# Kernel tuning notes

Measured on AMD Instinct MI355X. Metric: run time of the kernel, lower is better.

## Reference

```python
import jax, jax.numpy as jnp
import numpy as np
from jax import lax


def _conv(x, W, b):
    # x: [B,C,H,W], W: [O,I,3,3] -> [B,O,H,W], SAME padding, stride 1
    y = lax.conv_general_dilated(x, W, window_strides=(1, 1), padding='SAME',
                                 dimension_numbers=('NCHW', 'OIHW', 'NCHW'))
    return y + b[None, :, None, None]


def _cell(x, h, c, W, b):
    # Standard ConvLSTMCell: conv(concat(x,h)) -> 4*Hd gate channels (i,f,o,g)
    gates = _conv(jnp.concatenate([x, h], axis=1), W, b)
    ci, cf, co, cg = jnp.split(gates, 4, axis=1)
    i = jax.nn.sigmoid(ci)
    f = jax.nn.sigmoid(cf)
    o = jax.nn.sigmoid(co)
    g = jnp.tanh(cg)
    c_next = f * c + i * g
    h_next = o * jnp.tanh(c_next)
    return h_next, c_next


def setup_inputs() -> dict:
    key = jax.random.key(0)
    ks = jax.random.split(key, 4)
    B, T, C, H, W = 1, 32, 4, 128, 128
    Hd = 64
    x = jax.random.normal(ks[0], (B, T, C, H, W), dtype=jnp.float32)
    # small init scale to keep sigmoid/tanh out of deep saturation
    W0 = jax.random.normal(ks[1], (4 * Hd, C + Hd, 3, 3), dtype=jnp.float32) * 0.05
    b0 = jnp.zeros((4 * Hd,), dtype=jnp.float32)
    W1 = jax.random.normal(ks[2], (4 * Hd, Hd + Hd, 3, 3), dtype=jnp.float32) * 0.05
    b1 = jnp.zeros((4 * Hd,), dtype=jnp.float32)
    Wr = jax.random.normal(ks[3], (1, Hd, 3, 3), dtype=jnp.float32) * 0.05
    br = jnp.zeros((1,), dtype=jnp.float32)
    return {"x": x, "W0": W0, "b0": b0, "W1": W1, "b1": b1, "Wr": Wr, "br": br}


def reference(x, W0, b0, W1, b1, Wr, br):
    # Train mode with epsilon=1 (deterministic teacher forcing), hidden_state=None
    B, T, C, H, Wd = x.shape
    Hd = Wr.shape[1]
    zeros = jnp.zeros((B, Hd, H, Wd), dtype=x.dtype)
    carry0 = (zeros, zeros, zeros, zeros)  # (h0, c0, h1, c1)

    def step(carry, x_t):
        h0, c0, h1, c1 = carry
        h0, c0 = _cell(x_t, h0, c0, W0, b0)
        h1, c1 = _cell(h0, h1, c1, W1, b1)
        y = _conv(h1, Wr, br)  # [B,1,H,W]
        return (h0, c0, h1, c1), y[0]  # squeeze batch dim (B=1) -> [1,H,W]

    xs = jnp.transpose(x, (1, 0, 2, 3, 4))  # [T,B,C,H,W]
    _, ys = lax.scan(step, carry0, xs)
    return ys  # [T,1,H,W]
```

## Files before the change

kernel.cpp:

```cpp
#include <hip/hip_runtime.h>
#include <cstdint>
#include <cmath>

#define HW 128
#define NPIX (HW * HW)

typedef _Float16 half8 __attribute__((ext_vector_type(8)));
typedef _Float16 half4 __attribute__((ext_vector_type(4)));
typedef float floatx16 __attribute__((ext_vector_type(16)));
typedef unsigned long long u64;

__device__ __forceinline__ float sigf(float x) {
    return __builtin_amdgcn_rcpf(1.0f + __expf(-x));
}
__device__ __forceinline__ float tanhf_(float x) {
    float cx = fminf(fmaxf(x, -20.0f), 20.0f);
    float e2 = __expf(2.0f * cx);
    return (e2 - 1.0f) * __builtin_amdgcn_rcpf(e2 + 1.0f);
}

__device__ __forceinline__ half8 ld_coh(const _Float16* p) {
    union { u64 u[2]; half8 h; } cv;
    cv.u[0] = __hip_atomic_load((const u64*)p,
                                __ATOMIC_RELAXED, __HIP_MEMORY_SCOPE_AGENT);
    cv.u[1] = __hip_atomic_load((const u64*)p + 1,
                                __ATOMIC_RELAXED, __HIP_MEMORY_SCOPE_AGENT);
    return cv.h;
}

__device__ __forceinline__ void st_coh8(_Float16* p, half4 v) {
    asm volatile("global_store_dwordx2 %0, %1, off sc0 sc1"
                 :: "v"(p), "v"(v) : "memory");
}
__device__ __forceinline__ void st_coh4(float* p, float v) {
    asm volatile("global_store_dword %0, %1, off sc0 sc1"
                 :: "v"(p), "v"(v) : "memory");
}

__device__ __forceinline__ void group_sync(unsigned* gcnt, int g,
                                           int gy, int gx, unsigned k)
{
    asm volatile("s_waitcnt vmcnt(0)" ::: "memory");
    __syncthreads();
    const int tid = threadIdx.x;
    if (tid == 0)
        __hip_atomic_fetch_add(gcnt + g * 16, 1u,
                               __ATOMIC_RELAXED, __HIP_MEMORY_SCOPE_AGENT);
    if (tid < 9) {
        int dy = tid / 3 - 1, dx = tid % 3 - 1;
        int gy2 = gy + dy, gx2 = gx + dx;
        if (gy2 >= 0 && gy2 < 8 && gx2 >= 0 && gx2 < 4) {
            const unsigned* p = gcnt + (gy2 * 4 + gx2) * 16;
            while (__hip_atomic_load(p, __ATOMIC_RELAXED,
                                     __HIP_MEMORY_SCOPE_AGENT) < 8u * k)
                __builtin_amdgcn_s_sleep(1);
        }
    }
    __syncthreads();
}

template<int NKC, int CELL>
__device__ __forceinline__ void cell_phase(
    const _Float16* __restrict__ xt,
    const _Float16* __restrict__ hA,
    const _Float16* __restrict__ hB,
    const _Float16* wlds,
    const float* blds,
    float (&cr)[2][4],
    _Float16* __restrict__ hOut,
    _Float16* sbuf,
    const int (&spb)[3], const int (&slo)[3], int ch16,
    int y0, int x0, int s)
{
    const int tid  = threadIdx.x;
    const int lane = tid & 63;
    const int w    = tid >> 6;
    const int cl   = lane & 31;
    const int l5   = lane >> 5;

    half8 regs[NKC][3];
    #pragma unroll
    for (int kc = 0; kc < NKC; ++kc) {
        #pragma unroll
        for (int e0 = 0; e0 < 3; ++e0) {
            half8 v = {0, 0, 0, 0, 0, 0, 0, 0};
            const int pb = spb[e0];
            if (pb >= 0) {
                if (CELL == 0) {
                    if (kc == 0) { if (ch16 == 0) v = *(const half8*)(xt + (pb >> 3)); }
                    else v = ld_coh(hA + pb + (kc - 1) * 16);
                } else {
                    v = (kc < 4) ? ld_coh(hA + pb + kc * 16)
                                 : ld_coh(hB + pb + (kc - 4) * 16);
                }
            }
            regs[kc][e0] = v;
        }
    }

    floatx16 acc[2];
    #pragma unroll
    for (int p_ = 0; p_ < 2; ++p_)
        #pragma unroll
        for (int i = 0; i < 16; ++i) acc[p_][i] = 0.0f;

    __syncthreads();
    #pragma unroll
    for (int e0 = 0; e0 < 3; ++e0)
        if (slo[e0] >= 0) *(half8*)(sbuf + slo[e0]) = regs[0][e0];
    __syncthreads();

    const int r0 = 2 * w;
    #pragma unroll
    for (int kc = 0; kc < NKC; ++kc) {
        const _Float16* wk = wlds + (size_t)(kc * 9) * 512 + lane * 8;
        const _Float16* bbase = sbuf + ((size_t)((kc & 1) * 2 + l5) * 612) * 8;

        half8 bufA[3], bufB[3];
        #pragma unroll
        for (int d = 0; d < 3; ++d) {
            bufA[d] = *(const half8*)(bbase + ((r0    ) * 34 + cl + d) * 8);
            bufB[d] = *(const half8*)(bbase + ((r0 + 1) * 34 + cl + d) * 8);
        }
        #pragma unroll
        for (int dx = 0; dx < 3; ++dx) {
            half8 a = *(const half8*)(wk + dx * 512);
            acc[0] = __builtin_amdgcn_mfma_f32_32x32x16_f16(a, bufA[dx], acc[0], 0, 0, 0);
            acc[1] = __builtin_amdgcn_mfma_f32_32x32x16_f16(a, bufB[dx], acc[1], 0, 0, 0);
        }
        #pragma unroll
        for (int d = 0; d < 3; ++d)
            bufA[d] = *(const half8*)(bbase + ((r0 + 2) * 34 + cl + d) * 8);
        #pragma unroll
        for (int dx = 0; dx < 3; ++dx) {
            half8 a = *(const half8*)(wk + (3 + dx) * 512);
            acc[0] = __builtin_amdgcn_mfma_f32_32x32x16_f16(a, bufB[dx], acc[0], 0, 0, 0);
            acc[1] = __builtin_amdgcn_mfma_f32_32x32x16_f16(a, bufA[dx], acc[1], 0, 0, 0);
        }
        #pragma unroll
        for (int d = 0; d < 3; ++d)
            bufB[d] = *(const half8*)(bbase + ((r0 + 3) * 34 + cl + d) * 8);
        #pragma unroll
        for (int dx = 0; dx < 3; ++dx) {
            half8 a = *(const half8*)(wk + (6 + dx) * 512);
            acc[0] = __builtin_amdgcn_mfma_f32_32x32x16_f16(a, bufA[dx], acc[0], 0, 0, 0);
            acc[1] = __builtin_amdgcn_mfma_f32_32x32x16_f16(a, bufB[dx], acc[1], 0, 0, 0);
        }

        if (kc + 1 < NKC) {
            const int b = (kc + 1) & 1;
            #pragma unroll
            for (int e0 = 0; e0 < 3; ++e0)
                if (slo[e0] >= 0)
                    *(half8*)(sbuf + b * 9792 + slo[e0]) = regs[kc + 1][e0];
        }
        __syncthreads();
    }

    #pragma unroll
    for (int pos = 0; pos < 2; ++pos) {
        const int p  = 2 * w + pos;
        const int px = (y0 + p) * HW + x0 + cl;
        half4 hn;
        #pragma unroll
        for (int j = 0; j < 4; ++j) {
            const int bo = CELL * 32 + 4 * l5 + j;
            float iv = sigf(acc[pos][     j] + blds[bo]);
            float fv = sigf(acc[pos][ 4 + j] + blds[bo + 8]);
            float ov = sigf(acc[pos][ 8 + j] + blds[bo + 16]);
            float gv = tanhf_(acc[pos][12 + j] + blds[bo + 24]);
            float cv = fv * cr[pos][j] + iv * gv;
            cr[pos][j] = cv;
            hn[j] = (_Float16)(ov * tanhf_(cv));
        }
        st_coh8(hOut + (size_t)px * 64 + s * 8 + 4 * l5, hn);
    }
}

__device__ __forceinline__ void readout_phase(
    const half8 (&rv)[2], const float* wl, float brv,
    float* __restrict__ yout, _Float16* sbuf,
    const int (&rlo)[2], int yidx)
{
    const int tid = threadIdx.x;
    __syncthreads();
    #pragma unroll
    for (int e0 = 0; e0 < 2; ++e0)
        if (rlo[e0] >= 0) *(half8*)(sbuf + rlo[e0]) = rv[e0];
    __syncthreads();

    const int sub = tid & 7;
    const int p   = tid >> 3;
    const int pr  = p >> 3, pcc = p & 7;
    float sacc = 0.0f;
    #pragma unroll
    for (int dy = 0; dy < 3; ++dy)
        #pragma unroll
        for (int dx = 0; dx < 3; ++dx) {
            int pc = (pr + dy) * 10 + (pcc + dx);
            half8 hv = *(const half8*)(sbuf + ((size_t)pc * 8 + sub) * 8);
            int tap = dy * 3 + dx;
            #pragma unroll
            for (int j = 0; j < 8; ++j)
                sacc += wl[(sub * 8 + j) * 9 + tap] * (float)hv[j];
        }
    sacc += __shfl_xor(sacc, 1);
    sacc += __shfl_xor(sacc, 2);
    sacc += __shfl_xor(sacc, 4);
    if (sub == 0) st_coh4(yout + yidx, sacc + brv);
}

__global__ __launch_bounds__(512, 2)
void mega(const _Float16* __restrict__ xh, const _Float16* __restrict__ WpG,
          const float* __restrict__ b0g, const float* __restrict__ b1g,
          const float* __restrict__ Wr, const float* __restrict__ br,
          _Float16* __restrict__ h0a, _Float16* __restrict__ h0b,
          _Float16* __restrict__ h1a, _Float16* __restrict__ h1b,
          float* __restrict__ y, unsigned* gcnt)
{
    extern __shared__ __align__(16) char dyn[];
    _Float16* wlds = (_Float16*)dyn;
    _Float16* sbuf = (_Float16*)(dyn + 119808);
    float*    wl   = (float*)(dyn + 158976);
    float*    blds = (float*)(dyn + 161280);

    const int tid = threadIdx.x;
    const int bid = blockIdx.x;
    const int s = bid >> 5, g = bid & 31;
    const int ggy = g >> 2, ggx = g & 3;
    const int y0 = ggy * 16, x0 = ggx * 32;

    const half8* wsrc = (const half8*)(WpG + (size_t)s * 59904);
    for (int i = tid; i < 7488; i += 512) ((half8*)wlds)[i] = wsrc[i];
    for (int i = tid; i < 576; i += 512) wl[i] = Wr[i];
    if (tid < 64) {
        int cell = tid >> 5, gj = tid & 31;
        int gate = gj >> 3, h8 = gj & 7;
        blds[tid] = (cell ? b1g : b0g)[gate * 64 + s * 8 + h8];
    }
    const float brv = br[0];
    float c0r[2][4] = {{0, 0, 0, 0}, {0, 0, 0, 0}};
    float c1r[2][4] = {{0, 0, 0, 0}, {0, 0, 0, 0}};

    const int ch16 = tid & 1;
    int spb[3], slo[3];
    #pragma unroll
    for (int e0 = 0; e0 < 3; ++e0) {
        int e = tid + e0 * 512;
        spb[e0] = -1; slo[e0] = -1;
        if (e < 1224) {
            int pc = e >> 1;
            int r = pc / 34, c = pc - r * 34;
            int gy = y0 - 1 + r, gx = x0 - 1 + c;
            slo[e0] = (ch16 * 612 + pc) * 8;
            if (gy >= 0 && gy < HW && gx >= 0 && gx < HW)
                spb[e0] = (gy * HW + gx) * 64 + ch16 * 8;
        }
    }
    const int ch8 = tid & 7;
    const int py0 = y0 + (s >> 2) * 8, px0 = x0 + (s & 3) * 8;
    int rpb[2], rlo[2];
    #pragma unroll
    for (int e0 = 0; e0 < 2; ++e0) {
        int e = tid + e0 * 512;
        rpb[e0] = -1; rlo[e0] = -1;
        if (e < 800) {
            int pc = e >> 3;
            int r = pc / 10, c = pc - r * 10;
            int gy = py0 - 1 + r, gx = px0 - 1 + c;
            rlo[e0] = (pc * 8 + ch8) * 8;
            if (gy >= 0 && gy < HW && gx >= 0 && gx < HW)
                rpb[e0] = (gy * HW + gx) * 64 + ch8 * 8;
        }
    }
    const int yidx = (py0 + ((tid >> 3) >> 3)) * HW + px0 + ((tid >> 3) & 7);

    __syncthreads();

    #pragma unroll 1
    for (int t = 0; t < 32; ++t) {
        const _Float16* xt = xh + (size_t)t * NPIX * 8;
        _Float16* h0r = (t & 1) ? h0b : h0a;
        _Float16* h0w = (t & 1) ? h0a : h0b;
        _Float16* h1r = (t & 1) ? h1b : h1a;
        _Float16* h1w = (t & 1) ? h1a : h1b;

        cell_phase<5, 0>(xt, h0r, nullptr, wlds, blds, c0r, h0w, sbuf,
                         spb, slo, ch16, y0, x0, s);
        group_sync(gcnt, g, ggy, ggx, (unsigned)(t + 1));

        half8 rv[2];
        #pragma unroll
        for (int e0 = 0; e0 < 2; ++e0) {
            half8 v = {0, 0, 0, 0, 0, 0, 0, 0};
            if (rpb[e0] >= 0) v = ld_coh(h1r + rpb[e0]);
            rv[e0] = v;
        }

        cell_phase<8, 1>(nullptr, h0w, h1r, wlds + 23040, blds, c1r, h1w, sbuf,
                         spb, slo, ch16, y0, x0, s);
        if (t > 0) readout_phase(rv, wl, brv, y + (size_t)(t - 1) * NPIX, sbuf,
                                 rlo, yidx);
    }
    group_sync(gcnt, g, ggy, ggx, 33u);
    {
        half8 rv[2];
        #pragma unroll
        for (int e0 = 0; e0 < 2; ++e0) {
            half8 v = {0, 0, 0, 0, 0, 0, 0, 0};
            if (rpb[e0] >= 0) v = ld_coh(h1a + rpb[e0]);
            rv[e0] = v;
        }
        readout_phase(rv, wl, brv, y + (size_t)31 * NPIX, sbuf, rlo, yidx);
    }
}

__global__ void pack_w(const float* __restrict__ W, _Float16* __restrict__ Wp,
                       int NKC, int CIN_W, int cell1, int base, int total)
{
    int idx = blockIdx.x * 256 + threadIdx.x;
    if (idx >= total) return;
    int j = idx & 7, l = (idx >> 3) & 63;
    int rest = idx >> 9;
    int tap = rest % 9;
    int kt  = rest / 9;
    int kc = kt % NKC, s = kt / NKC;
    int rr = l & 31, l5 = l >> 5;
    int o = (rr >> 3) * 64 + s * 8 + (rr & 7);
    int k = kc * 16 + l5 * 8 + j;
    int cin = cell1 ? ((k < 4) ? k : ((k >= 16 && k < 80) ? k - 12 : -1)) : k;
    float v = (cin >= 0) ? W[((size_t)o * CIN_W + cin) * 9 + tap] : 0.0f;
    Wp[(size_t)s * 59904 + base + (size_t)(kc * 9 + tap) * 512 + l * 8 + j] = (_Float16)v;
}

__global__ void xconv(const float* __restrict__ x, _Float16* __restrict__ xh)
{
    int idx = blockIdx.x * 256 + threadIdx.x;
    int t = idx >> 14, px = idx & 16383;
    const float* xs = x + (size_t)t * 4 * NPIX + px;
    half8 v = {0, 0, 0, 0, 0, 0, 0, 0};
    v[0] = (_Float16)xs[0];
    v[1] = (_Float16)xs[NPIX];
    v[2] = (_Float16)xs[2 * NPIX];
    v[3] = (_Float16)xs[3 * NPIX];
    *(half8*)(xh + (size_t)idx * 8) = v;
}

extern "C" void kernel_launch(void* const* d_in, const int* in_sizes, int n_in,
                              void* d_out, int out_size, void* d_ws, size_t ws_size,
                              hipStream_t stream)
{
    const float* x  = (const float*)d_in[0];
    const float* W0 = (const float*)d_in[1];
    const float* b0 = (const float*)d_in[2];
    const float* W1 = (const float*)d_in[3];
    const float* b1 = (const float*)d_in[4];
    const float* Wr = (const float*)d_in[5];
    const float* br = (const float*)d_in[6];
    float* y = (float*)d_out;

    char* ws = (char*)d_ws;
    _Float16* h0a = (_Float16*)(ws);
    _Float16* h1a = (_Float16*)(ws + (2u << 20));
    _Float16* h0b = (_Float16*)(ws + (4u << 20));
    _Float16* h1b = (_Float16*)(ws + (6u << 20));
    _Float16* xh  = (_Float16*)(ws + (8u << 20));
    _Float16* WpG = (_Float16*)(ws + (16u << 20));
    unsigned* cnt = (unsigned*)(ws + (17u << 20));

    hipMemsetAsync(ws, 0, (4u << 20), stream);
    hipMemsetAsync(cnt, 0, 2048, stream);

    pack_w<<<dim3((184320 + 255) / 256), 256, 0, stream>>>(W0, WpG, 5, 68, 1, 0, 184320);
    pack_w<<<dim3((294912 + 255) / 256), 256, 0, stream>>>(W1, WpG, 8, 128, 0, 23040, 294912);
    xconv<<<dim3(2048), 256, 0, stream>>>(x, xh);

    hipFuncSetAttribute(reinterpret_cast<const void*>(mega),
                        hipFuncAttributeMaxDynamicSharedMemorySize, 161536);
    mega<<<dim3(256), 512, 161536, stream>>>(xh, WpG, b0, b1, Wr, br,
                                             h0a, h0b, h1a, h1b, y, cnt);
}
```

Baseline: 1.000 ms.

## Split layers into separate block families and pipeline them across timesteps

Launches twice as many blocks, with one family computing layer-0 cells and the other layer-1 cells plus the readout, offset by one timestep so the two layers run concurrently instead of back to back. Weights are no longer copied into LDS. Each k-chunk reads them straight from global memory, which shrinks shared memory enough to raise launch bounds to four blocks per CU. The per-chunk activation loads are software-pipelined one chunk ahead instead of all preloaded into registers. The cost is more global/L2 weight traffic per step and group syncs that now wait for sixteen arrivals, with correctness depending on the new buffer parity scheme and the resident-block assumption of the spin barrier.

Result: slower. 1.343 ms (+34.3%).

```diff
diff --git a/kernel.cpp b/kernel.cpp
--- a/kernel.cpp
+++ b/kernel.cpp
@@ -52,7 +52,7 @@
         if (gy2 >= 0 && gy2 < 8 && gx2 >= 0 && gx2 < 4) {
             const unsigned* p = gcnt + (gy2 * 4 + gx2) * 16;
             while (__hip_atomic_load(p, __ATOMIC_RELAXED,
-                                     __HIP_MEMORY_SCOPE_AGENT) < 8u * k)
+                                     __HIP_MEMORY_SCOPE_AGENT) < 16u * k)
                 __builtin_amdgcn_s_sleep(1);
         }
     }
@@ -64,7 +64,7 @@
     const _Float16* __restrict__ xt,
     const _Float16* __restrict__ hA,
     const _Float16* __restrict__ hB,
-    const _Float16* wlds,
+    const _Float16* __restrict__ wg,
     const float* blds,
     float (&cr)[2][4],
     _Float16* __restrict__ hOut,
@@ -78,9 +78,9 @@
     const int cl   = lane & 31;
     const int l5   = lane >> 5;
 
-    half8 regs[NKC][3];
-    #pragma unroll
-    for (int kc = 0; kc < NKC; ++kc) {
+    half8 vv[3];
+
+    auto stage_load = [&](int kc) {
         #pragma unroll
         for (int e0 = 0; e0 < 3; ++e0) {
             half8 v = {0, 0, 0, 0, 0, 0, 0, 0};
@@ -94,9 +94,16 @@
                                  : ld_coh(hB + pb + (kc - 4) * 16);
                 }
             }
-            regs[kc][e0] = v;
-        }
-    }
+            vv[e0] = v;
+        }
+    };
+    auto stage_write = [&](int b) {
+        #pragma unroll
+        for (int e0 = 0; e0 < 3; ++e0) {
+            if (slo[e0] >= 0)
+                *(half8*)(sbuf + b * 9792 + slo[e0]) = vv[e0];
+        }
+    };
 
     floatx16 acc[2];
     #pragma unroll
@@ -105,15 +112,21 @@
         for (int i = 0; i < 16; ++i) acc[p_][i] = 0.0f;
 
     __syncthreads();
-    #pragma unroll
-    for (int e0 = 0; e0 < 3; ++e0)
-        if (slo[e0] >= 0) *(half8*)(sbuf + slo[e0]) = regs[0][e0];
+    stage_load(0);
+    stage_write(0);
     __syncthreads();
 
     const int r0 = 2 * w;
-    #pragma unroll
+    #pragma unroll 1
     for (int kc = 0; kc < NKC; ++kc) {
-        const _Float16* wk = wlds + (size_t)(kc * 9) * 512 + lane * 8;
+        if (kc + 1 < NKC) stage_load(kc + 1);
+
+        half8 a[9];
+        const _Float16* wk = wg + (size_t)(kc * 9) * 512 + lane * 8;
+        #pragma unroll
+        for (int tap = 0; tap < 9; ++tap)
+            a[tap] = *(const half8*)(wk + tap * 512);
+
         const _Float16* bbase = sbuf + ((size_t)((kc & 1) * 2 + l5) * 612) * 8;
 
         half8 bufA[3], bufB[3];
@@ -124,36 +137,27 @@
         }
         #pragma unroll
         for (int dx = 0; dx < 3; ++dx) {
-            half8 a = *(const half8*)(wk + dx * 512);
-            acc[0] = __builtin_amdgcn_mfma_f32_32x32x16_f16(a, bufA[dx], acc[0], 0, 0, 0);
-            acc[1] = __builtin_amdgcn_mfma_f32_32x32x16_f16(a, bufB[dx], acc[1], 0, 0, 0);
+            acc[0] = __builtin_amdgcn_mfma_f32_32x32x16_f16(a[dx], bufA[dx], acc[0], 0, 0, 0);
+            acc[1] = __builtin_amdgcn_mfma_f32_32x32x16_f16(a[dx], bufB[dx], acc[1], 0, 0, 0);
         }
         #pragma unroll
         for (int d = 0; d < 3; ++d)
             bufA[d] = *(const half8*)(bbase + ((r0 + 2) * 34 + cl + d) * 8);
         #pragma unroll
         for (int dx = 0; dx < 3; ++dx) {
-            half8 a = *(const half8*)(wk + (3 + dx) * 512);
-            acc[0] = __builtin_amdgcn_mfma_f32_32x32x16_f16(a, bufB[dx], acc[0], 0, 0, 0);
-            acc[1] = __builtin_amdgcn_mfma_f32_32x32x16_f16(a, bufA[dx], acc[1], 0, 0, 0);
+            acc[0] = __builtin_amdgcn_mfma_f32_32x32x16_f16(a[3 + dx], bufB[dx], acc[0], 0, 0, 0);
+            acc[1] = __builtin_amdgcn_mfma_f32_32x32x16_f16(a[3 + dx], bufA[dx], acc[1], 0, 0, 0);
         }
         #pragma unroll
         for (int d = 0; d < 3; ++d)
             bufB[d] = *(const half8*)(bbase + ((r0 + 3) * 34 + cl + d) * 8);
         #pragma unroll
         for (int dx = 0; dx < 3; ++dx) {
-            half8 a = *(const half8*)(wk + (6 + dx) * 512);
-            acc[0] = __builtin_amdgcn_mfma_f32_32x32x16_f16(a, bufA[dx], acc[0], 0, 0, 0);
-            acc[1] = __builtin_amdgcn_mfma_f32_32x32x16_f16(a, bufB[dx], acc[1], 0, 0, 0);
-        }
-
-        if (kc + 1 < NKC) {
-            const int b = (kc + 1) & 1;
-            #pragma unroll
-            for (int e0 = 0; e0 < 3; ++e0)
-                if (slo[e0] >= 0)
-                    *(half8*)(sbuf + b * 9792 + slo[e0]) = regs[kc + 1][e0];
-        }
+            acc[0] = __builtin_amdgcn_mfma_f32_32x32x16_f16(a[6 + dx], bufA[dx], acc[0], 0, 0, 0);
+            acc[1] = __builtin_amdgcn_mfma_f32_32x32x16_f16(a[6 + dx], bufB[dx], acc[1], 0, 0, 0);
+        }
+
+        if (kc + 1 < NKC) stage_write((kc + 1) & 1);
         __syncthreads();
     }
 
@@ -210,7 +214,7 @@
     if (sub == 0) st_coh4(yout + yidx, sacc + brv);
 }
 
-__global__ __launch_bounds__(512, 2)
+__global__ __launch_bounds__(512, 4)
 void mega(const _Float16* __restrict__ xh, const _Float16* __restrict__ WpG,
           const float* __restrict__ b0g, const float* __restrict__ b1g,
           const float* __restrict__ Wr, const float* __restrict__ br,
@@ -219,19 +223,18 @@
           float* __restrict__ y, unsigned* gcnt)
 {
     extern __shared__ __align__(16) char dyn[];
-    _Float16* wlds = (_Float16*)dyn;
-    _Float16* sbuf = (_Float16*)(dyn + 119808);
-    float*    wl   = (float*)(dyn + 158976);
-    float*    blds = (float*)(dyn + 161280);
+    _Float16* sbuf = (_Float16*)dyn;
+    float*    wl   = (float*)(dyn + 39168);
+    float*    blds = (float*)(dyn + 41472);
 
     const int tid = threadIdx.x;
     const int bid = blockIdx.x;
-    const int s = bid >> 5, g = bid & 31;
-    const int ggy = g >> 2, ggx = g & 3;
+    const int grp = bid & 31;
+    const int fam = (bid >> 5) & 1;
+    const int s   = bid >> 6;
+    const int ggy = grp >> 2, ggx = grp & 3;
     const int y0 = ggy * 16, x0 = ggx * 32;
 
-    const half8* wsrc = (const half8*)(WpG + (size_t)s * 59904);
-    for (int i = tid; i < 7488; i += 512) ((half8*)wlds)[i] = wsrc[i];
     for (int i = tid; i < 576; i += 512) wl[i] = Wr[i];
     if (tid < 64) {
         int cell = tid >> 5, gj = tid & 31;
@@ -239,8 +242,9 @@
         blds[tid] = (cell ? b1g : b0g)[gate * 64 + s * 8 + h8];
     }
     const float brv = br[0];
-    float c0r[2][4] = {{0, 0, 0, 0}, {0, 0, 0, 0}};
-    float c1r[2][4] = {{0, 0, 0, 0}, {0, 0, 0, 0}};
+    float cr[2][4] = {{0, 0, 0, 0}, {0, 0, 0, 0}};
+
+    const _Float16* wg = WpG + (size_t)s * 59904 + (fam ? 23040 : 0);
 
     const int ch16 = tid & 1;
     int spb[3], slo[3];
@@ -278,37 +282,46 @@
     __syncthreads();
 
     #pragma unroll 1
-    for (int t = 0; t < 32; ++t) {
-        const _Float16* xt = xh + (size_t)t * NPIX * 8;
-        _Float16* h0r = (t & 1) ? h0b : h0a;
-        _Float16* h0w = (t & 1) ? h0a : h0b;
-        _Float16* h1r = (t & 1) ? h1b : h1a;
-        _Float16* h1w = (t & 1) ? h1a : h1b;
-
-        cell_phase<5, 0>(xt, h0r, nullptr, wlds, blds, c0r, h0w, sbuf,
-                         spb, slo, ch16, y0, x0, s);
-        group_sync(gcnt, g, ggy, ggx, (unsigned)(t + 1));
-
+    for (int tau = 0; tau <= 32; ++tau) {
+        if (fam == 0) {
+            if (tau < 32) {
+                const _Float16* xt = xh + (size_t)tau * NPIX * 8;
+                const _Float16* h0r = (tau & 1) ? h0a : h0b;
+                _Float16*       h0w = (tau & 1) ? h0b : h0a;
+                cell_phase<5, 0>(xt, h0r, nullptr, wg, blds, cr, h0w, sbuf,
+                                 spb, slo, ch16, y0, x0, s);
+            }
+        } else {
+            half8 rv[2];
+            if (tau >= 2) {
+                const _Float16* h1ro = (tau & 1) ? h1b : h1a;
+                #pragma unroll
+                for (int e0 = 0; e0 < 2; ++e0) {
+                    half8 v = {0, 0, 0, 0, 0, 0, 0, 0};
+                    if (rpb[e0] >= 0) v = ld_coh(h1ro + rpb[e0]);
+                    rv[e0] = v;
+                }
+            }
+            if (tau >= 1) {
+                const int t2 = tau - 1;
+                const _Float16* hAc = (t2 & 1) ? h0b : h0a;
+                const _Float16* hBc = (t2 & 1) ? h1a : h1b;
+                _Float16*       h1w = (t2 & 1) ? h1b : h1a;
+                cell_phase<8, 1>(nullptr, hAc, hBc, wg, blds, cr, h1w, sbuf,
+                                 spb, slo, ch16, y0, x0, s);
+            }
+            if (tau >= 2)
+                readout_phase(rv, wl, brv, y + (size_t)(tau - 2) * NPIX, sbuf,
+                              rlo, yidx);
+        }
+        group_sync(gcnt, grp, ggy, ggx, (unsigned)(tau + 1));
+    }
+    if (fam == 1) {
         half8 rv[2];
         #pragma unroll
         for (int e0 = 0; e0 < 2; ++e0) {
             half8 v = {0, 0, 0, 0, 0, 0, 0, 0};
-            if (rpb[e0] >= 0) v = ld_coh(h1r + rpb[e0]);
-            rv[e0] = v;
-        }
-
-        cell_phase<8, 1>(nullptr, h0w, h1r, wlds + 23040, blds, c1r, h1w, sbuf,
-                         spb, slo, ch16, y0, x0, s);
-        if (t > 0) readout_phase(rv, wl, brv, y + (size_t)(t - 1) * NPIX, sbuf,
-                                 rlo, yidx);
-    }
-    group_sync(gcnt, g, ggy, ggx, 33u);
-    {
-        half8 rv[2];
-        #pragma unroll
-        for (int e0 = 0; e0 < 2; ++e0) {
-            half8 v = {0, 0, 0, 0, 0, 0, 0, 0};
-            if (rpb[e0] >= 0) v = ld_coh(h1a + rpb[e0]);
+            if (rpb[e0] >= 0) v = ld_coh(h1b + rpb[e0]);
             rv[e0] = v;
         }
         readout_phase(rv, wl, brv, y + (size_t)31 * NPIX, sbuf, rlo, yidx);
@@ -368,7 +381,7 @@
     _Float16* WpG = (_Float16*)(ws + (16u << 20));
     unsigned* cnt = (unsigned*)(ws + (17u << 20));
 
-    hipMemsetAsync(ws, 0, (4u << 20), stream);
+    hipMemsetAsync(ws, 0, (8u << 20), stream);
     hipMemsetAsync(cnt, 0, 2048, stream);
 
     pack_w<<<dim3((184320 + 255) / 256), 256, 0, stream>>>(W0, WpG, 5, 68, 1, 0, 184320);
@@ -376,7 +389,7 @@
     xconv<<<dim3(2048), 256, 0, stream>>>(x, xh);
 
     hipFuncSetAttribute(reinterpret_cast<const void*>(mega),
-                        hipFuncAttributeMaxDynamicSharedMemorySize, 161536);
-    mega<<<dim3(256), 512, 161536, stream>>>(xh, WpG, b0, b1, Wr, br,
-                                             h0a, h0b, h1a, h1b, y, cnt);
-}
+                        hipFuncAttributeMaxDynamicSharedMemorySize, 41728);
+    mega<<<dim3(512), 512, 41728, stream>>>(xh, WpG, b0, b1, Wr, br,
+                                            h0a, h0b, h1a, h1b, y, cnt);
+}
```

## Prefetch next step's layer-0 inputs before readout, splitting loads from compute

Applied to the files above, without the earlier changes.

The cell phase is split into a load-issue function and a compute function. The layer-0 inputs for step t+1 (x and the freshly written h0 halo) are now loaded into registers before the readout phase of step t, so their global-load latency can overlap the readout work. The leading barrier in the readout phase is dropped to cut synchronisation. The trade-off is about 60 extra live VGPRs across the layer-1 phase, which may reduce occupancy or cause spills. Dropping the barrier could also open a shared-buffer race if the layer-1 phase does not end with its own barrier.

Result: slower. 1.106 ms (+10.6%).

```diff
diff --git a/kernel.cpp b/kernel.cpp
--- a/kernel.cpp
+++ b/kernel.cpp
@@ -60,25 +60,11 @@
 }
 
 template<int NKC, int CELL>
-__device__ __forceinline__ void cell_phase(
-    const _Float16* __restrict__ xt,
-    const _Float16* __restrict__ hA,
-    const _Float16* __restrict__ hB,
-    const _Float16* wlds,
-    const float* blds,
-    float (&cr)[2][4],
-    _Float16* __restrict__ hOut,
-    _Float16* sbuf,
-    const int (&spb)[3], const int (&slo)[3], int ch16,
-    int y0, int x0, int s)
-{
-    const int tid  = threadIdx.x;
-    const int lane = tid & 63;
-    const int w    = tid >> 6;
-    const int cl   = lane & 31;
-    const int l5   = lane >> 5;
-
-    half8 regs[NKC][3];
+__device__ __forceinline__ void issue_cell(
+    const _Float16* __restrict__ xt, const _Float16* __restrict__ hA,
+    const _Float16* __restrict__ hB, const int (&spb)[3], int ch16,
+    half8 (&regs)[NKC][3])
+{
     #pragma unroll
     for (int kc = 0; kc < NKC; ++kc) {
         #pragma unroll
@@ -97,6 +83,24 @@
             regs[kc][e0] = v;
         }
     }
+}
+
+template<int NKC, int CELL>
+__device__ __forceinline__ void cell_phase(
+    const half8 (&regs)[NKC][3],
+    const _Float16* wlds,
+    const float* blds,
+    float (&cr)[2][4],
+    _Float16* __restrict__ hOut,
+    _Float16* sbuf,
+    const int (&slo)[3],
+    int y0, int x0, int s)
+{
+    const int tid  = threadIdx.x;
+    const int lane = tid & 63;
+    const int w    = tid >> 6;
+    const int cl   = lane & 31;
+    const int l5   = lane >> 5;
 
     floatx16 acc[2];
     #pragma unroll
@@ -183,7 +187,6 @@
     const int (&rlo)[2], int yidx)
 {
     const int tid = threadIdx.x;
-    __syncthreads();
     #pragma unroll
     for (int e0 = 0; e0 < 2; ++e0)
         if (rlo[e0] >= 0) *(half8*)(sbuf + rlo[e0]) = rv[e0];
@@ -277,30 +280,42 @@
 
     __syncthreads();
 
+    half8 c1regs[5][3];
+    issue_cell<5, 0>(xh, h0a, nullptr, spb, ch16, c1regs);
+
     #pragma unroll 1
     for (int t = 0; t < 32; ++t) {
-        const _Float16* xt = xh + (size_t)t * NPIX * 8;
-        _Float16* h0r = (t & 1) ? h0b : h0a;
         _Float16* h0w = (t & 1) ? h0a : h0b;
         _Float16* h1r = (t & 1) ? h1b : h1a;
         _Float16* h1w = (t & 1) ? h1a : h1b;
 
-        cell_phase<5, 0>(xt, h0r, nullptr, wlds, blds, c0r, h0w, sbuf,
-                         spb, slo, ch16, y0, x0, s);
+        cell_phase<5, 0>(c1regs, wlds, blds, c0r, h0w, sbuf, slo, y0, x0, s);
         group_sync(gcnt, g, ggy, ggx, (unsigned)(t + 1));
 
         half8 rv[2];
-        #pragma unroll
-        for (int e0 = 0; e0 < 2; ++e0) {
-            half8 v = {0, 0, 0, 0, 0, 0, 0, 0};
-            if (rpb[e0] >= 0) v = ld_coh(h1r + rpb[e0]);
-            rv[e0] = v;
-        }
-
-        cell_phase<8, 1>(nullptr, h0w, h1r, wlds + 23040, blds, c1r, h1w, sbuf,
-                         spb, slo, ch16, y0, x0, s);
-        if (t > 0) readout_phase(rv, wl, brv, y + (size_t)(t - 1) * NPIX, sbuf,
-                                 rlo, yidx);
+        if (t > 0) {
+            #pragma unroll
+            for (int e0 = 0; e0 < 2; ++e0) {
+                half8 v = {0, 0, 0, 0, 0, 0, 0, 0};
+                if (rpb[e0] >= 0) v = ld_coh(h1r + rpb[e0]);
+                rv[e0] = v;
+            }
+        }
+
+        {
+            half8 c2regs[8][3];
+            issue_cell<8, 1>(nullptr, h0w, h1r, spb, ch16, c2regs);
+            cell_phase<8, 1>(c2regs, wlds + 23040, blds, c1r, h1w, sbuf,
+                             slo, y0, x0, s);
+        }
+
+        if (t + 1 < 32)
+            issue_cell<5, 0>(xh + (size_t)(t + 1) * NPIX * 8, h0w, nullptr,
+                             spb, ch16, c1regs);
+
+        if (t > 0)
+            readout_phase(rv, wl, brv, y + (size_t)(t - 1) * NPIX, sbuf,
+                          rlo, yidx);
     }
     group_sync(gcnt, g, ggy, ggx, 33u);
     {
```

## Double grid to 512 blocks with 8-row tiles and stream weights from global

Applied to the files above, without the earlier changes.

Spatial tiles shrink from 16 to 8 rows, so the persistent grid grows from 256 to 512 blocks, each wave computing one output row instead of two. Weights are no longer preloaded into LDS. They are streamed from global or L2 per channel chunk into registers with one-chunk-ahead prefetch, which cuts LDS use enough to fit more blocks per CU (launch bounds raised to 4). The goal is more parallelism and less per-block LDS pressure on the recurrent critical path. In exchange, weight traffic to L2 rises, each block does less reuse per weight load, and the neighbour group sync now covers 64 groups.

Measured after the change: 3.345 ms. 3.34x slower.

```diff
diff --git a/kernel.cpp b/kernel.cpp
--- a/kernel.cpp
+++ b/kernel.cpp
@@ -49,7 +49,7 @@
     if (tid < 9) {
         int dy = tid / 3 - 1, dx = tid % 3 - 1;
         int gy2 = gy + dy, gx2 = gx + dx;
-        if (gy2 >= 0 && gy2 < 8 && gx2 >= 0 && gx2 < 4) {
+        if (gy2 >= 0 && gy2 < 16 && gx2 >= 0 && gx2 < 4) {
             const unsigned* p = gcnt + (gy2 * 4 + gx2) * 16;
             while (__hip_atomic_load(p, __ATOMIC_RELAXED,
                                      __HIP_MEMORY_SCOPE_AGENT) < 8u * k)
@@ -64,12 +64,12 @@
     const _Float16* __restrict__ xt,
     const _Float16* __restrict__ hA,
     const _Float16* __restrict__ hB,
-    const _Float16* wlds,
+    const _Float16* __restrict__ wg,
     const float* blds,
-    float (&cr)[2][4],
+    float (&cr)[4],
     _Float16* __restrict__ hOut,
     _Float16* sbuf,
-    const int (&spb)[3], const int (&slo)[3], int ch16,
+    const int (&spb)[2], const int (&slo)[2], int ch16,
     int y0, int x0, int s)
 {
     const int tid  = threadIdx.x;
@@ -78,11 +78,10 @@
     const int cl   = lane & 31;
     const int l5   = lane >> 5;
 
-    half8 regs[NKC][3];
-    #pragma unroll
-    for (int kc = 0; kc < NKC; ++kc) {
-        #pragma unroll
-        for (int e0 = 0; e0 < 3; ++e0) {
+    half8 vv[2];
+    auto stage_load = [&](int kc) {
+        #pragma unroll
+        for (int e0 = 0; e0 < 2; ++e0) {
             half8 v = {0, 0, 0, 0, 0, 0, 0, 0};
             const int pb = spb[e0];
             if (pb >= 0) {
@@ -94,87 +93,71 @@
                                  : ld_coh(hB + pb + (kc - 4) * 16);
                 }
             }
-            regs[kc][e0] = v;
-        }
-    }
-
-    floatx16 acc[2];
-    #pragma unroll
-    for (int p_ = 0; p_ < 2; ++p_)
-        #pragma unroll
-        for (int i = 0; i < 16; ++i) acc[p_][i] = 0.0f;
-
-    __syncthreads();
-    #pragma unroll
-    for (int e0 = 0; e0 < 3; ++e0)
-        if (slo[e0] >= 0) *(half8*)(sbuf + slo[e0]) = regs[0][e0];
-    __syncthreads();
-
-    const int r0 = 2 * w;
+            vv[e0] = v;
+        }
+    };
+    auto stage_write = [&](int b) {
+        #pragma unroll
+        for (int e0 = 0; e0 < 2; ++e0)
+            if (slo[e0] >= 0) *(half8*)(sbuf + b * 5440 + slo[e0]) = vv[e0];
+    };
+
+    floatx16 acc;
+    #pragma unroll
+    for (int i = 0; i < 16; ++i) acc[i] = 0.0f;
+
+    half8 aP[9], aN[9];
+
+    __syncthreads();
+    stage_load(0);
+    stage_write(0);
+    {
+        const _Float16* wk = wg + lane * 8;
+        #pragma unroll
+        for (int tap = 0; tap < 9; ++tap)
+            aP[tap] = *(const half8*)(wk + tap * 512);
+    }
+    __syncthreads();
+
     #pragma unroll
     for (int kc = 0; kc < NKC; ++kc) {
-        const _Float16* wk = wlds + (size_t)(kc * 9) * 512 + lane * 8;
-        const _Float16* bbase = sbuf + ((size_t)((kc & 1) * 2 + l5) * 612) * 8;
-
-        half8 bufA[3], bufB[3];
-        #pragma unroll
-        for (int d = 0; d < 3; ++d) {
-            bufA[d] = *(const half8*)(bbase + ((r0    ) * 34 + cl + d) * 8);
-            bufB[d] = *(const half8*)(bbase + ((r0 + 1) * 34 + cl + d) * 8);
-        }
-        #pragma unroll
-        for (int dx = 0; dx < 3; ++dx) {
-            half8 a = *(const half8*)(wk + dx * 512);
-            acc[0] = __builtin_amdgcn_mfma_f32_32x32x16_f16(a, bufA[dx], acc[0], 0, 0, 0);
-            acc[1] = __builtin_amdgcn_mfma_f32_32x32x16_f16(a, bufB[dx], acc[1], 0, 0, 0);
-        }
-        #pragma unroll
-        for (int d = 0; d < 3; ++d)
-            bufA[d] = *(const half8*)(bbase + ((r0 + 2) * 34 + cl + d) * 8);
-        #pragma unroll
-        for (int dx = 0; dx < 3; ++dx) {
-            half8 a = *(const half8*)(wk + (3 + dx) * 512);
-            acc[0] = __builtin_amdgcn_mfma_f32_32x32x16_f16(a, bufB[dx], acc[0], 0, 0, 0);
-            acc[1] = __builtin_amdgcn_mfma_f32_32x32x16_f16(a, bufA[dx], acc[1], 0, 0, 0);
-        }
-        #pragma unroll
-        for (int d = 0; d < 3; ++d)
-            bufB[d] = *(const half8*)(bbase + ((r0 + 3) * 34 + cl + d) * 8);
-        #pragma unroll
-        for (int dx = 0; dx < 3; ++dx) {
-            half8 a = *(const half8*)(wk + (6 + dx) * 512);
-            acc[0] = __builtin_amdgcn_mfma_f32_32x32x16_f16(a, bufA[dx], acc[0], 0, 0, 0);
-            acc[1] = __builtin_amdgcn_mfma_f32_32x32x16_f16(a, bufB[dx], acc[1], 0, 0, 0);
-        }
-
         if (kc + 1 < NKC) {
-            const int b = (kc + 1) & 1;
-            #pragma unroll
-            for (int e0 = 0; e0 < 3; ++e0)
-                if (slo[e0] >= 0)
-                    *(half8*)(sbuf + b * 9792 + slo[e0]) = regs[kc + 1][e0];
+            stage_load(kc + 1);
+            const _Float16* wk = wg + (size_t)((kc + 1) * 9) * 512 + lane * 8;
+            #pragma unroll
+            for (int tap = 0; tap < 9; ++tap)
+                aN[tap] = *(const half8*)(wk + tap * 512);
+        }
+        const _Float16* bbase = sbuf + ((kc & 1) * 2 + l5) * 2720;
+        #pragma unroll
+        for (int dy = 0; dy < 3; ++dy)
+            #pragma unroll
+            for (int dx = 0; dx < 3; ++dx) {
+                half8 b = *(const half8*)(bbase + ((w + dy) * 34 + cl + dx) * 8);
+                acc = __builtin_amdgcn_mfma_f32_32x32x16_f16(aP[dy * 3 + dx], b, acc, 0, 0, 0);
+            }
+        if (kc + 1 < NKC) {
+            stage_write((kc + 1) & 1);
+            #pragma unroll
+            for (int tap = 0; tap < 9; ++tap) aP[tap] = aN[tap];
         }
         __syncthreads();
     }
 
-    #pragma unroll
-    for (int pos = 0; pos < 2; ++pos) {
-        const int p  = 2 * w + pos;
-        const int px = (y0 + p) * HW + x0 + cl;
-        half4 hn;
-        #pragma unroll
-        for (int j = 0; j < 4; ++j) {
-            const int bo = CELL * 32 + 4 * l5 + j;
-            float iv = sigf(acc[pos][     j] + blds[bo]);
-            float fv = sigf(acc[pos][ 4 + j] + blds[bo + 8]);
-            float ov = sigf(acc[pos][ 8 + j] + blds[bo + 16]);
-            float gv = tanhf_(acc[pos][12 + j] + blds[bo + 24]);
-            float cv = fv * cr[pos][j] + iv * gv;
-            cr[pos][j] = cv;
-            hn[j] = (_Float16)(ov * tanhf_(cv));
-        }
-        st_coh8(hOut + (size_t)px * 64 + s * 8 + 4 * l5, hn);
-    }
+    const int px = (y0 + w) * HW + x0 + cl;
+    half4 hn;
+    #pragma unroll
+    for (int j = 0; j < 4; ++j) {
+        const int bo = CELL * 32 + 4 * l5 + j;
+        float iv = sigf(acc[     j] + blds[bo]);
+        float fv = sigf(acc[ 4 + j] + blds[bo + 8]);
+        float ov = sigf(acc[ 8 + j] + blds[bo + 16]);
+        float gv = tanhf_(acc[12 + j] + blds[bo + 24]);
+        float cv = fv * cr[j] + iv * gv;
+        cr[j] = cv;
+        hn[j] = (_Float16)(ov * tanhf_(cv));
+    }
+    st_coh8(hOut + (size_t)px * 64 + s * 8 + 4 * l5, hn);
 }
 
 __device__ __forceinline__ void readout_phase(
@@ -183,34 +166,34 @@
     const int (&rlo)[2], int yidx)
 {
     const int tid = threadIdx.x;
-    __syncthreads();
     #pragma unroll
     for (int e0 = 0; e0 < 2; ++e0)
         if (rlo[e0] >= 0) *(half8*)(sbuf + rlo[e0]) = rv[e0];
     __syncthreads();
 
-    const int sub = tid & 7;
-    const int p   = tid >> 3;
-    const int pr  = p >> 3, pcc = p & 7;
-    float sacc = 0.0f;
-    #pragma unroll
-    for (int dy = 0; dy < 3; ++dy)
-        #pragma unroll
-        for (int dx = 0; dx < 3; ++dx) {
-            int pc = (pr + dy) * 10 + (pcc + dx);
-            half8 hv = *(const half8*)(sbuf + ((size_t)pc * 8 + sub) * 8);
-            int tap = dy * 3 + dx;
-            #pragma unroll
-            for (int j = 0; j < 8; ++j)
-                sacc += wl[(sub * 8 + j) * 9 + tap] * (float)hv[j];
-        }
-    sacc += __shfl_xor(sacc, 1);
-    sacc += __shfl_xor(sacc, 2);
-    sacc += __shfl_xor(sacc, 4);
-    if (sub == 0) st_coh4(yout + yidx, sacc + brv);
-}
-
-__global__ __launch_bounds__(512, 2)
+    if (tid < 256) {
+        const int sub = tid & 7;
+        const int p   = tid >> 3;
+        float sacc = 0.0f;
+        #pragma unroll
+        for (int dy = 0; dy < 3; ++dy)
+            #pragma unroll
+            for (int dx = 0; dx < 3; ++dx) {
+                int pc = dy * 34 + p + dx;
+                half8 hv = *(const half8*)(sbuf + ((size_t)pc * 8 + sub) * 8);
+                int tap = dy * 3 + dx;
+                #pragma unroll
+                for (int j = 0; j < 8; ++j)
+                    sacc += wl[(sub * 8 + j) * 9 + tap] * (float)hv[j];
+            }
+        sacc += __shfl_xor(sacc, 1);
+        sacc += __shfl_xor(sacc, 2);
+        sacc += __shfl_xor(sacc, 4);
+        if (sub == 0) st_coh4(yout + yidx, sacc + brv);
+    }
+}
+
+__global__ __launch_bounds__(512, 4)
 void mega(const _Float16* __restrict__ xh, const _Float16* __restrict__ WpG,
           const float* __restrict__ b0g, const float* __restrict__ b1g,
           const float* __restrict__ Wr, const float* __restrict__ br,
@@ -219,19 +202,16 @@
           float* __restrict__ y, unsigned* gcnt)
 {
     extern __shared__ __align__(16) char dyn[];
-    _Float16* wlds = (_Float16*)dyn;
-    _Float16* sbuf = (_Float16*)(dyn + 119808);
-    float*    wl   = (float*)(dyn + 158976);
-    float*    blds = (float*)(dyn + 161280);
+    _Float16* sbuf = (_Float16*)dyn;
+    float*    wl   = (float*)(dyn + 21760);
+    float*    blds = (float*)(dyn + 24064);
 
     const int tid = threadIdx.x;
     const int bid = blockIdx.x;
-    const int s = bid >> 5, g = bid & 31;
+    const int g = bid & 63, s = bid >> 6;
     const int ggy = g >> 2, ggx = g & 3;
-    const int y0 = ggy * 16, x0 = ggx * 32;
-
-    const half8* wsrc = (const half8*)(WpG + (size_t)s * 59904);
-    for (int i = tid; i < 7488; i += 512) ((half8*)wlds)[i] = wsrc[i];
+    const int y0 = ggy * 8, x0 = ggx * 32;
+
     for (int i = tid; i < 576; i += 512) wl[i] = Wr[i];
     if (tid < 64) {
         int cell = tid >> 5, gj = tid & 31;
@@ -239,68 +219,74 @@
         blds[tid] = (cell ? b1g : b0g)[gate * 64 + s * 8 + h8];
     }
     const float brv = br[0];
-    float c0r[2][4] = {{0, 0, 0, 0}, {0, 0, 0, 0}};
-    float c1r[2][4] = {{0, 0, 0, 0}, {0, 0, 0, 0}};
+    float c0r[4] = {0, 0, 0, 0};
+    float c1r[4] = {0, 0, 0, 0};
+
+    const _Float16* wg0 = WpG + (size_t)s * 59904;
+    const _Float16* wg1 = wg0 + 23040;
 
     const int ch16 = tid & 1;
-    int spb[3], slo[3];
-    #pragma unroll
-    for (int e0 = 0; e0 < 3; ++e0) {
+    int spb[2], slo[2];
+    #pragma unroll
+    for (int e0 = 0; e0 < 2; ++e0) {
         int e = tid + e0 * 512;
         spb[e0] = -1; slo[e0] = -1;
-        if (e < 1224) {
+        if (e < 680) {
             int pc = e >> 1;
             int r = pc / 34, c = pc - r * 34;
             int gy = y0 - 1 + r, gx = x0 - 1 + c;
-            slo[e0] = (ch16 * 612 + pc) * 8;
+            slo[e0] = (ch16 * 340 + pc) * 8;
             if (gy >= 0 && gy < HW && gx >= 0 && gx < HW)
                 spb[e0] = (gy * HW + gx) * 64 + ch16 * 8;
         }
     }
     const int ch8 = tid & 7;
-    const int py0 = y0 + (s >> 2) * 8, px0 = x0 + (s & 3) * 8;
     int rpb[2], rlo[2];
     #pragma unroll
     for (int e0 = 0; e0 < 2; ++e0) {
         int e = tid + e0 * 512;
         rpb[e0] = -1; rlo[e0] = -1;
-        if (e < 800) {
+        if (e < 816) {
             int pc = e >> 3;
-            int r = pc / 10, c = pc - r * 10;
-            int gy = py0 - 1 + r, gx = px0 - 1 + c;
+            int r = pc / 34, c = pc - r * 34;
+            int gy = y0 + s - 1 + r, gx = x0 - 1 + c;
             rlo[e0] = (pc * 8 + ch8) * 8;
             if (gy >= 0 && gy < HW && gx >= 0 && gx < HW)
                 rpb[e0] = (gy * HW + gx) * 64 + ch8 * 8;
         }
     }
-    const int yidx = (py0 + ((tid >> 3) >> 3)) * HW + px0 + ((tid >> 3) & 7);
+    const int yidx = (y0 + s) * HW + x0 + (tid >> 3);
 
     __syncthreads();
 
     #pragma unroll 1
     for (int t = 0; t < 32; ++t) {
         const _Float16* xt = xh + (size_t)t * NPIX * 8;
-        _Float16* h0r = (t & 1) ? h0b : h0a;
-        _Float16* h0w = (t & 1) ? h0a : h0b;
-        _Float16* h1r = (t & 1) ? h1b : h1a;
-        _Float16* h1w = (t & 1) ? h1a : h1b;
-
-        cell_phase<5, 0>(xt, h0r, nullptr, wlds, blds, c0r, h0w, sbuf,
+        const _Float16* h0r = (t & 1) ? h0b : h0a;
+        _Float16*       h0w = (t & 1) ? h0a : h0b;
+        const _Float16* h1r = (t & 1) ? h1b : h1a;
+        _Float16*       h1w = (t & 1) ? h1a : h1b;
+
+        cell_phase<5, 0>(xt, h0r, nullptr, wg0, blds, c0r, h0w, sbuf,
                          spb, slo, ch16, y0, x0, s);
         group_sync(gcnt, g, ggy, ggx, (unsigned)(t + 1));
 
         half8 rv[2];
-        #pragma unroll
-        for (int e0 = 0; e0 < 2; ++e0) {
-            half8 v = {0, 0, 0, 0, 0, 0, 0, 0};
-            if (rpb[e0] >= 0) v = ld_coh(h1r + rpb[e0]);
-            rv[e0] = v;
-        }
-
-        cell_phase<8, 1>(nullptr, h0w, h1r, wlds + 23040, blds, c1r, h1w, sbuf,
+        if (t > 0) {
+            #pragma unroll
+            for (int e0 = 0; e0 < 2; ++e0) {
+                half8 v = {0, 0, 0, 0, 0, 0, 0, 0};
+                if (rpb[e0] >= 0) v = ld_coh(h1r + rpb[e0]);
+                rv[e0] = v;
+            }
+        }
+
+        cell_phase<8, 1>(nullptr, h0w, h1r, wg1, blds, c1r, h1w, sbuf,
                          spb, slo, ch16, y0, x0, s);
-        if (t > 0) readout_phase(rv, wl, brv, y + (size_t)(t - 1) * NPIX, sbuf,
-                                 rlo, yidx);
+
+        if (t > 0)
+            readout_phase(rv, wl, brv, y + (size_t)(t - 1) * NPIX, sbuf,
+                          rlo, yidx);
     }
     group_sync(gcnt, g, ggy, ggx, 33u);
     {
@@ -369,14 +355,14 @@
     unsigned* cnt = (unsigned*)(ws + (17u << 20));
 
     hipMemsetAsync(ws, 0, (4u << 20), stream);
-    hipMemsetAsync(cnt, 0, 2048, stream);
+    hipMemsetAsync(cnt, 0, 4096, stream);
 
     pack_w<<<dim3((184320 + 255) / 256), 256, 0, stream>>>(W0, WpG, 5, 68, 1, 0, 184320);
     pack_w<<<dim3((294912 + 255) / 256), 256, 0, stream>>>(W1, WpG, 8, 128, 0, 23040, 294912);
     xconv<<<dim3(2048), 256, 0, stream>>>(x, xh);
 
     hipFuncSetAttribute(reinterpret_cast<const void*>(mega),
-                        hipFuncAttributeMaxDynamicSharedMemorySize, 161536);
-    mega<<<dim3(256), 512, 161536, stream>>>(xh, WpG, b0, b1, Wr, br,
-                                             h0a, h0b, h1a, h1b, y, cnt);
-}
+                        hipFuncAttributeMaxDynamicSharedMemorySize, 24320);
+    mega<<<dim3(512), 512, 24320, stream>>>(xh, WpG, b0, b1, Wr, br,
+                                            h0a, h0b, h1a, h1b, y, cnt);
+}
```
